# Kernel tuning notes

Hardware: AMD Instinct MI355X
Metric: run time of the kernel (lower is better)

The kernel has to match this reference:

```python
import jax, jax.numpy as jnp
import numpy as np

WORLD_SIZE = 8
M_LOCAL = 1024   # max_M // world_size
K = 4096
N = 4096


def setup_inputs() -> dict:
    key = jax.random.key(0)
    k1, k2 = jax.random.split(key)
    # Each rank's local activation shard: [world_size, M_local, K]
    A_shards = jax.random.normal(k1, (WORLD_SIZE, M_LOCAL, K), dtype=jnp.float32)
    # weight stored [N, K] (transed_weight = False path)
    weight = jax.random.normal(k2, (N, K), dtype=jnp.float32) * 0.02
    return {"A_shards": A_shards, "weight": weight, "transed_weight": 0}


def reference(A_shards, weight, transed_weight):
    # All-gather: concatenate rank shards along M -> [max_M, K]
    ws, m_local, k = A_shards.shape
    A_full = A_shards.reshape(ws * m_local, k)
    # GEMM: weight is [N, K] when transed_weight is falsy, [K, N] otherwise
    W = weight if transed_weight else weight.T  # -> [K, N]
    out = jnp.matmul(A_full, W)  # [max_M, N]
    return out
```

## Files before the change

### kernel.cpp

```cpp
#include <hip/hip_runtime.h>
#include <hip/hip_bf16.h>

#define M_TOTAL 8192
#define KDIM    4096
#define NDIM    4096

#define BM 256
#define BN 256
#define BK 32
#define NT (KDIM / BK)
#define AREG (BM * BK)
#define BREG (BN * BK)
#define BUFE (AREG + BREG)

typedef __bf16 bf16x8 __attribute__((ext_vector_type(8)));
typedef float  f32x4  __attribute__((ext_vector_type(4)));

__device__ __forceinline__ unsigned short f32_to_bf16_rne(unsigned u) {
    unsigned r = u + 0x7fffu + ((u >> 16) & 1u);
    return (unsigned short)(r >> 16);
}

__device__ __forceinline__ void cvt8(const float* __restrict__ s,
                                     unsigned short* __restrict__ d) {
    const uint4* sp = (const uint4*)s;
    uint4 x = sp[0];
    uint4 y = sp[1];
    uint4 o;
    o.x = (unsigned)f32_to_bf16_rne(x.x) | ((unsigned)f32_to_bf16_rne(x.y) << 16);
    o.y = (unsigned)f32_to_bf16_rne(x.z) | ((unsigned)f32_to_bf16_rne(x.w) << 16);
    o.z = (unsigned)f32_to_bf16_rne(y.x) | ((unsigned)f32_to_bf16_rne(y.y) << 16);
    o.w = (unsigned)f32_to_bf16_rne(y.z) | ((unsigned)f32_to_bf16_rne(y.w) << 16);
    *(uint4*)d = o;
}

__global__ __launch_bounds__(256) void cvt_both(const float* __restrict__ A,
                                                unsigned short* __restrict__ Abf,
                                                long nA,
                                                const float* __restrict__ W,
                                                unsigned short* __restrict__ Wbf) {
    long i = ((long)blockIdx.x * 256 + threadIdx.x) * 8;
    if (i < nA) {
        cvt8(A + i, Abf + i);
    } else {
        long j = i - nA;
        cvt8(W + j, Wbf + j);
    }
}

__device__ __forceinline__ void gload_lds16(const unsigned short* g, unsigned short* l) {
    __builtin_amdgcn_global_load_lds(
        (const __attribute__((address_space(1))) unsigned int*)g,
        (__attribute__((address_space(3))) unsigned int*)l,
        16, 0, 0);
}

__global__ __launch_bounds__(512, 2) void gemm_bt(const unsigned short* __restrict__ A,
                                                  const unsigned short* __restrict__ B,
                                                  float* __restrict__ C) {
    extern __shared__ unsigned short smem[];

    const int tid  = threadIdx.x;
    const int wave = tid >> 6;
    const int lane = tid & 63;

    const int n0 = blockIdx.x * BN;
    const int m0 = blockIdx.y * BM;

    const int rsub = tid >> 2;
    const int cswz = (tid & 3) ^ ((tid >> 3) & 3);
    const unsigned short* pA0 = A + (size_t)(m0 + rsub)       * KDIM + cswz * 8;
    const unsigned short* pA1 = A + (size_t)(m0 + 128 + rsub) * KDIM + cswz * 8;
    const unsigned short* pB0 = B + (size_t)(n0 + rsub)       * KDIM + cswz * 8;
    const unsigned short* pB1 = B + (size_t)(n0 + 128 + rsub) * KDIM + cswz * 8;
    const int woff = wave * 512;

    const int wm   = wave >> 2;
    const int wn   = wave & 3;
    const int quad = lane >> 4;
    const int r    = lane & 15;
    const int sidx = (quad ^ ((r >> 1) & 3)) * 8;

    int aoff[8], boff[4];
#pragma unroll
    for (int mi = 0; mi < 8; ++mi) aoff[mi] = (wm * 128 + mi * 16 + r) * BK + sidx;
#pragma unroll
    for (int ni = 0; ni < 4; ++ni) boff[ni] = (wn * 64 + ni * 16 + r) * BK + sidx;

    f32x4 acc[8][4] = {};

#define SAp(b) (smem + (b) * BUFE)
#define SBq(b) (smem + (b) * BUFE + AREG)
#define STAGE(TS, SB) do {                                                  \
        const size_t so_ = (size_t)(TS) * BK;                               \
        gload_lds16(pA0 + so_, SAp(SB) + woff);                             \
        gload_lds16(pA1 + so_, SAp(SB) + 4096 + woff);                      \
        gload_lds16(pB0 + so_, SBq(SB) + woff);                             \
        gload_lds16(pB1 + so_, SBq(SB) + 4096 + woff);                      \
    } while (0)

    STAGE(0, 0);
    STAGE(1, 1);
    STAGE(2, 2);

#define GITER(RB, SB, VM, DOSTAGE, TS) do {                                 \
        asm volatile("s_waitcnt vmcnt(" #VM ")" ::: "memory");              \
        __builtin_amdgcn_s_barrier();                                       \
        asm volatile("" ::: "memory");                                      \
        if (DOSTAGE) STAGE(TS, SB);                                         \
        bf16x8 aF[8], bF[4];                                                \
        _Pragma("unroll")                                                   \
        for (int mi = 0; mi < 8; ++mi)                                      \
            aF[mi] = *(const bf16x8*)(SAp(RB) + aoff[mi]);                  \
        _Pragma("unroll")                                                   \
        for (int ni = 0; ni < 4; ++ni)                                      \
            bF[ni] = *(const bf16x8*)(SBq(RB) + boff[ni]);                  \
        __builtin_amdgcn_s_setprio(1);                                      \
        _Pragma("unroll")                                                   \
        for (int mi = 0; mi < 8; ++mi)                                      \
            _Pragma("unroll")                                               \
            for (int ni = 0; ni < 4; ++ni)                                  \
                acc[mi][ni] = __builtin_amdgcn_mfma_f32_16x16x32_bf16(      \
                    aF[mi], bF[ni], acc[mi][ni], 0, 0, 0);                  \
        __builtin_amdgcn_s_setprio(0);                                      \
        asm volatile("s_waitcnt lgkmcnt(0)" ::: "memory");                  \
    } while (0)

    for (int g = 0; g < NT / 4 - 1; ++g) {
        const int t = g * 4;
        GITER(0, 3, 8, true, t + 3);
        GITER(1, 0, 8, true, t + 4);
        GITER(2, 1, 8, true, t + 5);
        GITER(3, 2, 8, true, t + 6);
    }
    GITER(0, 3, 8, true, 127);
    GITER(1, 0, 8, false, 0);
    GITER(2, 1, 4, false, 0);
    GITER(3, 2, 0, false, 0);

#undef GITER
#undef STAGE
#undef SAp
#undef SBq

#pragma unroll
    for (int mi = 0; mi < 8; ++mi) {
        const int row = m0 + wm * 128 + mi * 16 + quad * 4;
#pragma unroll
        for (int ni = 0; ni < 4; ++ni) {
            const int col = n0 + wn * 64 + ni * 16 + r;
            float* p = C + (size_t)row * NDIM + col;
#pragma unroll
            for (int rr = 0; rr < 4; ++rr)
                p[(size_t)rr * NDIM] = acc[mi][ni][rr];
        }
    }
}

extern "C" void kernel_launch(void* const* d_in, const int* in_sizes, int n_in,
                              void* d_out, int out_size, void* d_ws, size_t ws_size,
                              hipStream_t stream) {
    const float* A = (const float*)d_in[0];
    const float* W = (const float*)d_in[1];
    float* out = (float*)d_out;

    unsigned short* Abf = (unsigned short*)d_ws;
    unsigned short* Wbf = Abf + (size_t)M_TOTAL * KDIM;

    const long nA = (long)M_TOTAL * KDIM;
    const long nW = (long)NDIM * KDIM;
    const long nTot = nA + nW;

    cvt_both<<<(int)(nTot / 8 / 256), 256, 0, stream>>>(A, Abf, nA, W, Wbf);

    static bool attr_done = false;
    if (!attr_done) {
        hipFuncSetAttribute((const void*)gemm_bt,
                            hipFuncAttributeMaxDynamicSharedMemorySize, 128 * 1024);
        attr_done = true;
    }

    dim3 grid(NDIM / BN, M_TOTAL / BM);
    gemm_bt<<<grid, 512, 128 * 1024, stream>>>(Abf, Wbf, out);
}
```

Measured before the change: 488.5 us.

## Software-pipeline LDS fragment reads one k-tile ahead of MFMA compute

Double-buffers the register fragments so that each iteration reads the next k-tile's A/B fragments from LDS while the MFMAs run on the fragments loaded in the previous iteration. A sched_barrier separates the reads from the MFMAs, and the vmcnt waits are tightened because the data must be resident one tile earlier. The goal is to hide LDS read latency behind matrix-core work. In exchange it doubles fragment register usage (48 extra VGPRs), which could cause spills under the 512x2 launch bounds, and it shortens the effective global-load prefetch depth.

Result: slower. 623.6 us (+27.7%).

```diff
diff --git a/kernel.cpp b/kernel.cpp
--- a/kernel.cpp
+++ b/kernel.cpp
@@ -88,6 +88,7 @@
     for (int ni = 0; ni < 4; ++ni) boff[ni] = (wn * 64 + ni * 16 + r) * BK + sidx;
 
     f32x4 acc[8][4] = {};
+    bf16x8 aF0[8], bF0[4], aF1[8], bF1[4];
 
 #define SAp(b) (smem + (b) * BUFE)
 #define SBq(b) (smem + (b) * BUFE + AREG)
@@ -99,46 +100,62 @@
         gload_lds16(pB1 + so_, SBq(SB) + 4096 + woff);                      \
     } while (0)
 
-    STAGE(0, 0);
-    STAGE(1, 1);
-    STAGE(2, 2);
-
-#define GITER(RB, SB, VM, DOSTAGE, TS) do {                                 \
-        asm volatile("s_waitcnt vmcnt(" #VM ")" ::: "memory");              \
-        __builtin_amdgcn_s_barrier();                                       \
-        asm volatile("" ::: "memory");                                      \
-        if (DOSTAGE) STAGE(TS, SB);                                         \
-        bf16x8 aF[8], bF[4];                                                \
+#define READF(RB, AF, BF) do {                                              \
+        const unsigned short* baA_ = SAp(RB);                               \
+        const unsigned short* baB_ = SBq(RB);                               \
         _Pragma("unroll")                                                   \
         for (int mi = 0; mi < 8; ++mi)                                      \
-            aF[mi] = *(const bf16x8*)(SAp(RB) + aoff[mi]);                  \
+            AF[mi] = *(const bf16x8*)(baA_ + aoff[mi]);                     \
         _Pragma("unroll")                                                   \
         for (int ni = 0; ni < 4; ++ni)                                      \
-            bF[ni] = *(const bf16x8*)(SBq(RB) + boff[ni]);                  \
+            BF[ni] = *(const bf16x8*)(baB_ + boff[ni]);                     \
+    } while (0)
+
+#define MFMAC(AF, BF) do {                                                  \
         __builtin_amdgcn_s_setprio(1);                                      \
         _Pragma("unroll")                                                   \
         for (int mi = 0; mi < 8; ++mi)                                      \
             _Pragma("unroll")                                               \
             for (int ni = 0; ni < 4; ++ni)                                  \
                 acc[mi][ni] = __builtin_amdgcn_mfma_f32_16x16x32_bf16(      \
-                    aF[mi], bF[ni], acc[mi][ni], 0, 0, 0);                  \
+                    AF[mi], BF[ni], acc[mi][ni], 0, 0, 0);                  \
         __builtin_amdgcn_s_setprio(0);                                      \
+    } while (0)
+
+#define ITER(RBn, SB, VM, DOSTAGE, TS, AFc, BFc, AFn, BFn) do {             \
+        asm volatile("s_waitcnt vmcnt(" #VM ")" ::: "memory");              \
+        __builtin_amdgcn_s_barrier();                                       \
+        asm volatile("" ::: "memory");                                      \
+        if (DOSTAGE) STAGE(TS, SB);                                         \
+        READF(RBn, AFn, BFn);                                               \
+        __builtin_amdgcn_sched_barrier(0);                                  \
+        MFMAC(AFc, BFc);                                                    \
         asm volatile("s_waitcnt lgkmcnt(0)" ::: "memory");                  \
     } while (0)
+
+    STAGE(0, 0);
+    STAGE(1, 1);
+    STAGE(2, 2);
+    asm volatile("s_waitcnt vmcnt(8)" ::: "memory");
+    __builtin_amdgcn_s_barrier();
+    asm volatile("" ::: "memory");
+    READF(0, aF0, bF0);
 
     for (int g = 0; g < NT / 4 - 1; ++g) {
         const int t = g * 4;
-        GITER(0, 3, 8, true, t + 3);
-        GITER(1, 0, 8, true, t + 4);
-        GITER(2, 1, 8, true, t + 5);
-        GITER(3, 2, 8, true, t + 6);
-    }
-    GITER(0, 3, 8, true, 127);
-    GITER(1, 0, 8, false, 0);
-    GITER(2, 1, 4, false, 0);
-    GITER(3, 2, 0, false, 0);
-
-#undef GITER
+        ITER(1, 3, 4, true, t + 3, aF0, bF0, aF1, bF1);
+        ITER(2, 0, 4, true, t + 4, aF1, bF1, aF0, bF0);
+        ITER(3, 1, 4, true, t + 5, aF0, bF0, aF1, bF1);
+        ITER(0, 2, 4, true, t + 6, aF1, bF1, aF0, bF0);
+    }
+    ITER(1, 3, 4, true, 127, aF0, bF0, aF1, bF1);
+    ITER(2, 0, 4, false, 0, aF1, bF1, aF0, bF0);
+    ITER(3, 1, 0, false, 0, aF0, bF0, aF1, bF1);
+    MFMAC(aF1, bF1);
+
+#undef ITER
+#undef MFMAC
+#undef READF
 #undef STAGE
 #undef SAp
 #undef SBq
```

## Switch GEMM to BK=64 double-buffered pipeline with quadrant-split LDS reads

Applied to the files above, without the earlier changes.

Replaces the 4-stage BK=32 LDS ring with a 2-stage double buffer of BK=64 tiles, using an 8-way XOR swizzle for the wider rows. Each K tile is processed as four quadrant MFMA groups, with LDS fragment reads interleaved between barriers so that reads overlap with matrix math. The aim is fewer barriers per unit of K and better overlap of ds_reads with MFMA. The tradeoffs are a shallower global prefetch depth (one tile ahead) and extra barriers inside each tile body.

After: 495.5 us. No clear change (+1.4%).

```diff
diff --git a/kernel.cpp b/kernel.cpp
--- a/kernel.cpp
+++ b/kernel.cpp
@@ -5,13 +5,8 @@
 #define KDIM    4096
 #define NDIM    4096
 
-#define BM 256
-#define BN 256
-#define BK 32
-#define NT (KDIM / BK)
-#define AREG (BM * BK)
-#define BREG (BN * BK)
-#define BUFE (AREG + BREG)
+#define BK 64
+#define NTT 64
 
 typedef __bf16 bf16x8 __attribute__((ext_vector_type(8)));
 typedef float  f32x4  __attribute__((ext_vector_type(4)));
@@ -64,84 +59,125 @@
     const int wave = tid >> 6;
     const int lane = tid & 63;
 
-    const int n0 = blockIdx.x * BN;
-    const int m0 = blockIdx.y * BM;
-
-    const int rsub = tid >> 2;
-    const int cswz = (tid & 3) ^ ((tid >> 3) & 3);
-    const unsigned short* pA0 = A + (size_t)(m0 + rsub)       * KDIM + cswz * 8;
-    const unsigned short* pA1 = A + (size_t)(m0 + 128 + rsub) * KDIM + cswz * 8;
-    const unsigned short* pB0 = B + (size_t)(n0 + rsub)       * KDIM + cswz * 8;
-    const unsigned short* pB1 = B + (size_t)(n0 + 128 + rsub) * KDIM + cswz * 8;
+    const int n0 = blockIdx.x * 256;
+    const int m0 = blockIdx.y * 256;
+
+    const int srow = tid >> 3;
+    const int sg8  = ((tid & 7) ^ ((tid >> 3) & 7)) * 8;
+    const unsigned short* gA = A + (size_t)(m0 + srow) * KDIM + sg8;
+    const unsigned short* gB = B + (size_t)(n0 + srow) * KDIM + sg8;
     const int woff = wave * 512;
 
     const int wm   = wave >> 2;
     const int wn   = wave & 3;
     const int quad = lane >> 4;
     const int r    = lane & 15;
-    const int sidx = (quad ^ ((r >> 1) & 3)) * 8;
-
-    int aoff[8], boff[4];
-#pragma unroll
-    for (int mi = 0; mi < 8; ++mi) aoff[mi] = (wm * 128 + mi * 16 + r) * BK + sidx;
-#pragma unroll
-    for (int ni = 0; ni < 4; ++ni) boff[ni] = (wn * 64 + ni * 16 + r) * BK + sidx;
+
+    int aoff[16], boff[8];
+#pragma unroll
+    for (int mi = 0; mi < 8; ++mi)
+#pragma unroll
+        for (int s = 0; s < 2; ++s) {
+            const int row = wm * 128 + mi * 16 + r;
+            aoff[mi * 2 + s] = row * 64 + (((s * 4 + quad) ^ (row & 7)) * 8);
+        }
+#pragma unroll
+    for (int ni = 0; ni < 4; ++ni)
+#pragma unroll
+        for (int s = 0; s < 2; ++s) {
+            const int row = wn * 64 + ni * 16 + r;
+            boff[ni * 2 + s] = row * 64 + (((s * 4 + quad) ^ (row & 7)) * 8);
+        }
 
     f32x4 acc[8][4] = {};
-
-#define SAp(b) (smem + (b) * BUFE)
-#define SBq(b) (smem + (b) * BUFE + AREG)
-#define STAGE(TS, SB) do {                                                  \
-        const size_t so_ = (size_t)(TS) * BK;                               \
-        gload_lds16(pA0 + so_, SAp(SB) + woff);                             \
-        gload_lds16(pA1 + so_, SAp(SB) + 4096 + woff);                      \
-        gload_lds16(pB0 + so_, SBq(SB) + woff);                             \
-        gload_lds16(pB1 + so_, SBq(SB) + 4096 + woff);                      \
-    } while (0)
-
-    STAGE(0, 0);
-    STAGE(1, 1);
-    STAGE(2, 2);
-
-#define GITER(RB, SB, VM, DOSTAGE, TS) do {                                 \
-        asm volatile("s_waitcnt vmcnt(" #VM ")" ::: "memory");              \
-        __builtin_amdgcn_s_barrier();                                       \
-        asm volatile("" ::: "memory");                                      \
-        if (DOSTAGE) STAGE(TS, SB);                                         \
-        bf16x8 aF[8], bF[4];                                                \
+    bf16x8 aT[8], aB_[8], bL[4], bR[4];
+
+#define ABUF(d) (smem + (d) * 32768)
+#define BBUF(d) (smem + (d) * 32768 + 16384)
+#define SGA(d, T, H) do {                                                   \
+        const unsigned short* g_ = gA + (size_t)(T) * BK + (size_t)(H) * 128 * KDIM; \
+        gload_lds16(g_,                     ABUF(d) + (H) * 8192 + woff);   \
+        gload_lds16(g_ + (size_t)64 * KDIM, ABUF(d) + (H) * 8192 + 4096 + woff); \
+    } while (0)
+#define SGB(d, T, H) do {                                                   \
+        const unsigned short* g_ = gB + (size_t)(T) * BK + (size_t)(H) * 128 * KDIM; \
+        gload_lds16(g_,                     BBUF(d) + (H) * 8192 + woff);   \
+        gload_lds16(g_ + (size_t)64 * KDIM, BBUF(d) + (H) * 8192 + 4096 + woff); \
+    } while (0)
+#define STAGEFULL(d, T) do { SGA(d, T, 0); SGA(d, T, 1);                    \
+                             SGB(d, T, 0); SGB(d, T, 1); } while (0)
+#define RDA(F, d, half) do {                                                \
         _Pragma("unroll")                                                   \
-        for (int mi = 0; mi < 8; ++mi)                                      \
-            aF[mi] = *(const bf16x8*)(SAp(RB) + aoff[mi]);                  \
+        for (int j = 0; j < 8; ++j)                                         \
+            F[j] = *(const bf16x8*)(ABUF(d) + aoff[(half) * 8 + j]);        \
+    } while (0)
+#define RDB(F, d, nh) do {                                                  \
         _Pragma("unroll")                                                   \
-        for (int ni = 0; ni < 4; ++ni)                                      \
-            bF[ni] = *(const bf16x8*)(SBq(RB) + boff[ni]);                  \
+        for (int j = 0; j < 4; ++j)                                         \
+            F[j] = *(const bf16x8*)(BBUF(d) + boff[(nh) * 4 + j]);          \
+    } while (0)
+#define QD(AF, BF, MH, NH) do {                                             \
         __builtin_amdgcn_s_setprio(1);                                      \
         _Pragma("unroll")                                                   \
-        for (int mi = 0; mi < 8; ++mi)                                      \
+        for (int mi = 0; mi < 4; ++mi)                                      \
             _Pragma("unroll")                                               \
-            for (int ni = 0; ni < 4; ++ni)                                  \
-                acc[mi][ni] = __builtin_amdgcn_mfma_f32_16x16x32_bf16(      \
-                    aF[mi], bF[ni], acc[mi][ni], 0, 0, 0);                  \
+            for (int ni = 0; ni < 2; ++ni)                                  \
+                _Pragma("unroll")                                           \
+                for (int s = 0; s < 2; ++s)                                 \
+                    acc[(MH) * 4 + mi][(NH) * 2 + ni] =                     \
+                        __builtin_amdgcn_mfma_f32_16x16x32_bf16(            \
+                            AF[mi * 2 + s], BF[ni * 2 + s],                 \
+                            acc[(MH) * 4 + mi][(NH) * 2 + ni], 0, 0, 0);    \
         __builtin_amdgcn_s_setprio(0);                                      \
-        asm volatile("s_waitcnt lgkmcnt(0)" ::: "memory");                  \
-    } while (0)
-
-    for (int g = 0; g < NT / 4 - 1; ++g) {
-        const int t = g * 4;
-        GITER(0, 3, 8, true, t + 3);
-        GITER(1, 0, 8, true, t + 4);
-        GITER(2, 1, 8, true, t + 5);
-        GITER(3, 2, 8, true, t + 6);
-    }
-    GITER(0, 3, 8, true, 127);
-    GITER(1, 0, 8, false, 0);
-    GITER(2, 1, 4, false, 0);
-    GITER(3, 2, 0, false, 0);
-
-#undef GITER
-#undef STAGE
-#undef SAp
-#undef SBq
+    } while (0)
+#define FEN asm volatile("" ::: "memory")
+#define BARX do { FEN; __builtin_amdgcn_s_barrier(); FEN; } while (0)
+#define LG0  asm volatile("s_waitcnt lgkmcnt(0)" ::: "memory")
+#define VMW(N) asm volatile("s_waitcnt vmcnt(" #N ")" ::: "memory")
+
+#define TILEBODY(d) do {                                                    \
+         RDA(aT, d, 0); RDB(bL, d, 0);                               \
+                BARX; LG0; QD(aT, bL, 0, 0); BARX;                          \
+         RDB(bR, d, 1);                                              \
+                BARX; LG0; QD(aT, bR, 0, 1); BARX;                          \
+         RDA(aB_, d, 1);                                             \
+                BARX; LG0; QD(aB_, bL, 1, 0); BARX;                         \
+         QD(aB_, bR, 1, 1);                                          \
+    } while (0)
+
+    STAGEFULL(0, 0);
+
+    for (int i = 0; i < 31; ++i) {
+        STAGEFULL(1, 2 * i + 1);
+        VMW(8);
+        BARX;
+        TILEBODY(0);
+        STAGEFULL(0, 2 * i + 2);
+        VMW(8);
+        BARX;
+        TILEBODY(1);
+    }
+    STAGEFULL(1, 63);
+    VMW(8);
+    BARX;
+    TILEBODY(0);
+    VMW(0);
+    BARX;
+    TILEBODY(1);
+
+#undef TILEBODY
+#undef VMW
+#undef LG0
+#undef BARX
+#undef FEN
+#undef QD
+#undef RDB
+#undef RDA
+#undef STAGEFULL
+#undef SGB
+#undef SGA
+#undef BBUF
+#undef ABUF
 
 #pragma unroll
     for (int mi = 0; mi < 8; ++mi) {
@@ -180,6 +216,6 @@
         attr_done = true;
     }
 
-    dim3 grid(NDIM / BN, M_TOTAL / BM);
+    dim3 grid(NDIM / 256, M_TOTAL / 256);
     gemm_bt<<<grid, 512, 128 * 1024, stream>>>(Abf, Wbf, out);
 }
```
